# Performance work log

Measured on AMD Instinct MI355X. Metric: run time of the kernel, lower is better.

The kernel has to match this reference:

```python
import jax, jax.numpy as jnp
import numpy as np

K = 2  # top-k experts per token


def setup_inputs() -> dict:
    key = jax.random.key(0)
    k1, k2 = jax.random.split(key)
    B, T, D, E = 4, 4096, 4096, 64
    x = jax.random.normal(k1, (B, T, D), dtype=jnp.float32)
    W = jax.random.normal(k2, (E, D), dtype=jnp.float32) * (1.0 / np.sqrt(D))
    return {"x": x, "W": W}


def reference(x, W):
    # router_logits: [B, T, E]  (nn.Linear with no bias: x @ W.T)
    router_logits = jnp.einsum('btd,ed->bte', x, W)
    # top-k over expert dim, then softmax over the k selected logits
    topk_logits, topk_idx = jax.lax.top_k(router_logits, K)  # [B,T,K]
    topk_weight = jax.nn.softmax(topk_logits, axis=-1)       # [B,T,K]
    return (topk_idx, topk_weight, router_logits)
```

## Files before the change

kernel.cpp:

```cpp
#include <hip/hip_runtime.h>
#include <math.h>

#define NTOK 16384
#define DDIM 4096
#define NEXP 64
#define TAU  2e-4f
#define WS_LO 262144
#define NCW  32

typedef short bf16x8 __attribute__((ext_vector_type(8)));
typedef float f32x4  __attribute__((ext_vector_type(4)));

__device__ __forceinline__ unsigned short bf16_rne(float f) {
  unsigned u = __float_as_uint(f);
  u += 0x7fffu + ((u >> 16) & 1u);
  return (unsigned short)(u >> 16);
}

__device__ __forceinline__ void split4(float4 v, uint2& hi, uint2& lo) {
  unsigned h0 = bf16_rne(v.x), h1 = bf16_rne(v.y), h2 = bf16_rne(v.z), h3 = bf16_rne(v.w);
  float r0 = v.x - __uint_as_float(h0 << 16);
  float r1 = v.y - __uint_as_float(h1 << 16);
  float r2 = v.z - __uint_as_float(h2 << 16);
  float r3 = v.w - __uint_as_float(h3 << 16);
  unsigned l0 = bf16_rne(r0), l1 = bf16_rne(r1), l2 = bf16_rne(r2), l3 = bf16_rne(r3);
  hi = make_uint2(h0 | (h1 << 16), h2 | (h3 << 16));
  lo = make_uint2(l0 | (l1 << 16), l2 | (l3 << 16));
}

__device__ __forceinline__ bf16x8 mk8(uint2 a, uint2 b) {
  union { uint4 u; bf16x8 v; } t;
  t.u = make_uint4(a.x, a.y, b.x, b.y);
  return t.v;
}

__device__ __forceinline__ void gld_lds16(const float* g, char* l) {
  __builtin_amdgcn_global_load_lds((const __attribute__((address_space(1))) void*)g,
                                   (__attribute__((address_space(3))) void*)l,
                                   16, 0, 0);
}

__device__ __forceinline__ bool better(float va, int ia, float vb, int ib) {
  return (va > vb) || (va == vb && ia < ib);
}
__device__ __forceinline__ bool betterd(double va, int ia, double vb, int ib) {
  return (va > vb) || (va == vb && ia < ib);
}
#define CE(va, ia, vb, ib) { if (better(vb, ib, va, ia)) { float _tv = va; va = vb; vb = _tv; int _ti = ia; ia = ib; ib = _ti; } }

__global__ __launch_bounds__(256)
void presplit_w(const float* __restrict__ w, short* __restrict__ ws) {
  const int tid = blockIdx.x * 256 + threadIdx.x;
  const int e = tid >> 9;
  const int o = tid & 511;
  const int c = o >> 2, q = o & 3;
  const int l = (e & 15) + 16 * q;
  const int g = e >> 4;
  const float* src = w + (size_t)e * DDIM + o * 8;
  float4 v0 = *(const float4*)src;
  float4 v1 = *(const float4*)(src + 4);
  uint2 h0, s0, h1, s1;
  split4(v0, h0, s0);
  split4(v1, h1, s1);
  const int off = c * 2048 + g * 512 + l * 8;
  *(uint4*)(ws + off)         = make_uint4(h0.x, h0.y, h1.x, h1.y);
  *(uint4*)(ws + WS_LO + off) = make_uint4(s0.x, s0.y, s1.x, s1.y);
}

__device__ __noinline__ void fixup_token(const float* __restrict__ x,
                                         const float* __restrict__ wgt,
                                         float* __restrict__ out_idx,
                                         float* __restrict__ out_wt,
                                         int tok, unsigned pk, int l) {
  const int e0 = pk & 255, e1 = (pk >> 8) & 255, e2 = (pk >> 16) & 255, e3 = (pk >> 24) & 255;
  const float* xr = x   + (size_t)tok * DDIM + l * 64;
  const float* w0 = wgt + (size_t)e0 * DDIM + l * 64;
  const float* w1 = wgt + (size_t)e1 * DDIM + l * 64;
  const float* w2 = wgt + (size_t)e2 * DDIM + l * 64;
  const float* w3 = wgt + (size_t)e3 * DDIM + l * 64;
  double s0 = 0.0, s1 = 0.0, s2 = 0.0, s3 = 0.0;
#pragma unroll 4
  for (int j = 0; j < 64; j += 4) {
    float4 xv = *(const float4*)(xr + j);
    float4 av = *(const float4*)(w0 + j);
    s0 = fma((double)xv.x, (double)av.x, s0); s0 = fma((double)xv.y, (double)av.y, s0);
    s0 = fma((double)xv.z, (double)av.z, s0); s0 = fma((double)xv.w, (double)av.w, s0);
    av = *(const float4*)(w1 + j);
    s1 = fma((double)xv.x, (double)av.x, s1); s1 = fma((double)xv.y, (double)av.y, s1);
    s1 = fma((double)xv.z, (double)av.z, s1); s1 = fma((double)xv.w, (double)av.w, s1);
    av = *(const float4*)(w2 + j);
    s2 = fma((double)xv.x, (double)av.x, s2); s2 = fma((double)xv.y, (double)av.y, s2);
    s2 = fma((double)xv.z, (double)av.z, s2); s2 = fma((double)xv.w, (double)av.w, s2);
    av = *(const float4*)(w3 + j);
    s3 = fma((double)xv.x, (double)av.x, s3); s3 = fma((double)xv.y, (double)av.y, s3);
    s3 = fma((double)xv.z, (double)av.z, s3); s3 = fma((double)xv.w, (double)av.w, s3);
  }
#pragma unroll
  for (int m = 1; m < 64; m <<= 1) {
    s0 += __shfl_xor(s0, m);
    s1 += __shfl_xor(s1, m);
    s2 += __shfl_xor(s2, m);
    s3 += __shfl_xor(s3, m);
  }
  if (l == 0) {
    double v0 = s0, v1 = s1, v2 = s2, v3 = s3;
    int i0 = e0, i1 = e1, i2 = e2, i3 = e3;
    if (betterd(v1, i1, v0, i0)) { double tv = v0; v0 = v1; v1 = tv; int ti = i0; i0 = i1; i1 = ti; }
    if (betterd(v3, i3, v2, i2)) { double tv = v2; v2 = v3; v3 = tv; int ti = i2; i2 = i3; i3 = ti; }
    if (betterd(v2, i2, v0, i0)) { double tv = v0; v0 = v2; v2 = tv; int ti = i0; i0 = i2; i2 = ti; }
    if (betterd(v3, i3, v1, i1)) { double tv = v1; v1 = v3; v3 = tv; int ti = i1; i1 = i3; i3 = ti; }
    if (betterd(v2, i2, v1, i1)) { double tv = v1; v1 = v2; v2 = tv; int ti = i1; i1 = i2; i2 = ti; }
    double ex = exp(v1 - v0);
    double den = 1.0 + ex;
    out_idx[tok * 2 + 0] = (float)i0;
    out_idx[tok * 2 + 1] = (float)i1;
    out_wt[tok * 2 + 0]  = (float)(1.0 / den);
    out_wt[tok * 2 + 1]  = (float)(ex / den);
  }
}

__global__ __launch_bounds__(256, 2)
void router_main(const float* __restrict__ x, const float* __restrict__ wgt,
                 const short* __restrict__ ws, float* __restrict__ out) {
  __shared__ __align__(16) char ldsbuf[65536];

  const int u = threadIdx.x;
  const int l = u & 63;
  const int wid = u >> 6;
  const int tokBase = blockIdx.x * 32;
  const int row = l & 15;
  const int hq = l >> 4;

  char* ring = ldsbuf + wid * 16384;

  const float* xb0 = x + (size_t)(tokBase +  0 + row) * DDIM + wid * 1024 +  0 + hq * 4;
  const float* xb1 = x + (size_t)(tokBase +  0 + row) * DDIM + wid * 1024 + 16 + hq * 4;
  const float* xb2 = x + (size_t)(tokBase + 16 + row) * DDIM + wid * 1024 +  0 + hq * 4;
  const float* xb3 = x + (size_t)(tokBase + 16 + row) * DDIM + wid * 1024 + 16 + hq * 4;

  const short* whp = ws + wid * 65536 + l * 8;

  const int dsoff = (hq >> 1) * 1024 + ((hq & 1) * 32 + row) * 16;

  f32x4 acc[2][4];
#pragma unroll
  for (int tt = 0; tt < 2; ++tt)
#pragma unroll
    for (int g = 0; g < 4; ++g) acc[tt][g] = (f32x4){0.f, 0.f, 0.f, 0.f};

  bf16x8 whA[4], wlA[4], whB[4], wlB[4];

#define LDW(WH, WL, cc)                                                        \
  { _Pragma("unroll")                                                          \
    for (int g = 0; g < 4; ++g) {                                              \
      WH[g] = *(const bf16x8*)(whp + (cc) * 2048 + g * 512);                   \
      WL[g] = *(const bf16x8*)(whp + WS_LO + (cc) * 2048 + g * 512);           \
    } }

  gld_lds16(xb0, ring);
  gld_lds16(xb1, ring + 1024);
  gld_lds16(xb2, ring + 2048);
  gld_lds16(xb3, ring + 3072);
  asm volatile("" ::: "memory");
  LDW(whA, wlA, 0)
  asm volatile("" ::: "memory");
  gld_lds16(xb0 + 32, ring + 4096);
  gld_lds16(xb1 + 32, ring + 4096 + 1024);
  gld_lds16(xb2 + 32, ring + 4096 + 2048);
  gld_lds16(xb3 + 32, ring + 4096 + 3072);
  asm volatile("" ::: "memory");
  LDW(whB, wlB, 1)

  int slr = 0;
  int slw = 2;

#define STEP(S, WH, WL)                                                        \
  {                                                                            \
    asm volatile("" ::: "memory");                                             \
    const int chx = (S) + 2;                                                   \
    char* xdst = ring + ((chx < NCW) ? slw : 3) * 4096;                        \
    const int xofs = ((chx < NCW) ? chx : (NCW - 1)) * 32;                     \
    gld_lds16(xb0 + xofs, xdst);                                               \
    gld_lds16(xb1 + xofs, xdst + 1024);                                        \
    gld_lds16(xb2 + xofs, xdst + 2048);                                        \
    gld_lds16(xb3 + xofs, xdst + 3072);                                        \
    asm volatile("s_waitcnt vmcnt(16)" ::: "memory");                          \
    const char* rb = ring + slr * 4096;                                        \
    {                                                                          \
      float4 f0 = *(const float4*)(rb + dsoff);                                \
      float4 f1 = *(const float4*)(rb + dsoff + 256);                          \
      uint2 h0, s0, h1, s1;                                                    \
      split4(f0, h0, s0); split4(f1, h1, s1);                                  \
      bf16x8 ahi = mk8(h0, h1), alo = mk8(s0, s1);                             \
      _Pragma("unroll")                                                        \
      for (int g = 0; g < 4; ++g) {                                            \
        acc[0][g] = __builtin_amdgcn_mfma_f32_16x16x32_bf16(ahi, WH[g], acc[0][g], 0, 0, 0); \
        acc[0][g] = __builtin_amdgcn_mfma_f32_16x16x32_bf16(ahi, WL[g], acc[0][g], 0, 0, 0); \
        acc[0][g] = __builtin_amdgcn_mfma_f32_16x16x32_bf16(alo, WH[g], acc[0][g], 0, 0, 0); \
      }                                                                        \
    }                                                                          \
    {                                                                          \
      float4 f0 = *(const float4*)(rb + 2048 + dsoff);                         \
      float4 f1 = *(const float4*)(rb + 2048 + dsoff + 256);                   \
      uint2 h0, s0, h1, s1;                                                    \
      split4(f0, h0, s0); split4(f1, h1, s1);                                  \
      bf16x8 ahi = mk8(h0, h1), alo = mk8(s0, s1);                             \
      _Pragma("unroll")                                                        \
      for (int g = 0; g < 4; ++g) {                                            \
        acc[1][g] = __builtin_amdgcn_mfma_f32_16x16x32_bf16(ahi, WH[g], acc[1][g], 0, 0, 0); \
        acc[1][g] = __builtin_amdgcn_mfma_f32_16x16x32_bf16(ahi, WL[g], acc[1][g], 0, 0, 0); \
        acc[1][g] = __builtin_amdgcn_mfma_f32_16x16x32_bf16(alo, WH[g], acc[1][g], 0, 0, 0); \
      }                                                                        \
    }                                                                          \
    const int chw = ((S) + 2 < NCW) ? (S) + 2 : (NCW - 1);                     \
    asm volatile("" ::: "memory");                                             \
    LDW(WH, WL, chw)                                                           \
    slr = (slr == 2) ? 0 : slr + 1;                                            \
    slw = (slw == 2) ? 0 : slw + 1;                                            \
  }

  for (int s = 0; s < NCW; s += 2) {
    STEP(s, whA, wlA)
    STEP(s + 1, whB, wlB)
  }

  __syncthreads();
  float* p = (float*)ldsbuf;
#define PIDX(KQ, TT, G, R) ((((((KQ) * 2 + (TT)) * 4 + (G)) * 4 + (R)) << 6) + l)
#pragma unroll
  for (int tt = 0; tt < 2; ++tt)
#pragma unroll
    for (int g = 0; g < 4; ++g)
#pragma unroll
      for (int r = 0; r < 4; ++r)
        p[PIDX(wid, tt, g, r)] = acc[tt][g][r];
  __syncthreads();

  float* out_idx = out;
  float* out_wt  = out + NTOK * 2;
  float* out_lg  = out + NTOK * 4;

#pragma unroll
  for (int tt = 0; tt < 2; ++tt) {
    float v0 = p[PIDX(0, tt, 0, wid)] + p[PIDX(1, tt, 0, wid)] + p[PIDX(2, tt, 0, wid)] + p[PIDX(3, tt, 0, wid)];
    float v1 = p[PIDX(0, tt, 1, wid)] + p[PIDX(1, tt, 1, wid)] + p[PIDX(2, tt, 1, wid)] + p[PIDX(3, tt, 1, wid)];
    float v2 = p[PIDX(0, tt, 2, wid)] + p[PIDX(1, tt, 2, wid)] + p[PIDX(2, tt, 2, wid)] + p[PIDX(3, tt, 2, wid)];
    float v3 = p[PIDX(0, tt, 3, wid)] + p[PIDX(1, tt, 3, wid)] + p[PIDX(2, tt, 3, wid)] + p[PIDX(3, tt, 3, wid)];

    const int tok = tokBase + tt * 16 + (l >> 4) * 4 + wid;
    {
      float* dst = out_lg + (size_t)tok * NEXP + (l & 15);
      dst[0]  = v0;
      dst[16] = v1;
      dst[32] = v2;
      dst[48] = v3;
    }

    const int cbase = (l & 15);
    int i0 = cbase, i1 = cbase + 16, i2 = cbase + 32, i3 = cbase + 48;
    CE(v0, i0, v1, i1) CE(v2, i2, v3, i3) CE(v0, i0, v2, i2) CE(v1, i1, v3, i3) CE(v1, i1, v2, i2)
#pragma unroll
    for (int m = 1; m <= 8; m <<= 1) {
      float p0 = __shfl_xor(v0, m), p1 = __shfl_xor(v1, m);
      float p2 = __shfl_xor(v2, m), p3 = __shfl_xor(v3, m);
      int j0 = __shfl_xor(i0, m), j1 = __shfl_xor(i1, m);
      int j2 = __shfl_xor(i2, m), j3 = __shfl_xor(i3, m);
      CE(v0, i0, p3, j3) CE(v1, i1, p2, j2) CE(v2, i2, p1, j1) CE(v3, i3, p0, j0)
      CE(v0, i0, v2, i2) CE(v1, i1, v3, i3) CE(v0, i0, v1, i1) CE(v2, i2, v3, i3)
    }

    bool flag = false;
    unsigned pk = 0;
    if (cbase == 0) {
      flag = (v0 - v1 < TAU) || (v1 - v2 < TAU) || (v2 - v3 < TAU);
      pk = (unsigned)i0 | ((unsigned)i1 << 8) | ((unsigned)i2 << 16) | ((unsigned)i3 << 24);
      if (!flag) {
        float ex = expf(v1 - v0);
        float den = 1.0f + ex;
        out_idx[tok * 2 + 0] = (float)i0;
        out_idx[tok * 2 + 1] = (float)i1;
        out_wt[tok * 2 + 0]  = 1.0f / den;
        out_wt[tok * 2 + 1]  = ex / den;
      }
    }
    unsigned long long mk = __ballot(flag);
    while (mk) {
      const int src = __builtin_ctzll(mk);
      mk &= mk - 1;
      const unsigned pks = (unsigned)__shfl((int)pk, src);
      fixup_token(x, wgt, out_idx, out_wt, tokBase + tt * 16 + (src >> 4) * 4 + wid, pks, l);
    }
  }
}

extern "C" void kernel_launch(void* const* d_in, const int* in_sizes, int n_in,
                              void* d_out, int out_size, void* d_ws, size_t ws_size,
                              hipStream_t stream) {
  const float* x = (const float*)d_in[0];
  const float* w = (const float*)d_in[1];
  float* out = (float*)d_out;
  short* ws = (short*)d_ws;

  hipLaunchKernelGGL(presplit_w, dim3(128), dim3(256), 0, stream, w, ws);
  hipLaunchKernelGGL(router_main, dim3(NTOK / 32), dim3(256), 0, stream, x, w, ws, out);
}
```

Measured before the change: 88.04 us.

## Deepen x/W prefetch pipeline to three chunks and stagger K-start per block

Extends the software pipeline from two to three chunks in flight, using a 4-slot LDS ring and four sets of weight registers, with the wait threshold raised to match. It also rotates each block's starting K chunk by a per-block offset, so concurrent blocks read different parts of W and x at the same moment. The aim is to hide more global-load latency and spread memory traffic across channels. The cost is higher register pressure from the extra weight buffers, which could hurt occupancy under launch_bounds(256,2). Past the end, prefetches wrap around and reload real chunks that are never used.

```diff
diff --git a/kernel.cpp b/kernel.cpp
--- a/kernel.cpp
+++ b/kernel.cpp
@@ -133,6 +133,9 @@
 
   char* ring = ldsbuf + wid * 16384;
 
+  const int P = (blockIdx.x * 13) & 31;
+#define PHYS(T) (((T) + P) & 31)
+
   const float* xb0 = x + (size_t)(tokBase +  0 + row) * DDIM + wid * 1024 +  0 + hq * 4;
   const float* xb1 = x + (size_t)(tokBase +  0 + row) * DDIM + wid * 1024 + 16 + hq * 4;
   const float* xb2 = x + (size_t)(tokBase + 16 + row) * DDIM + wid * 1024 +  0 + hq * 4;
@@ -148,44 +151,42 @@
 #pragma unroll
     for (int g = 0; g < 4; ++g) acc[tt][g] = (f32x4){0.f, 0.f, 0.f, 0.f};
 
-  bf16x8 whA[4], wlA[4], whB[4], wlB[4];
-
-#define LDW(WH, WL, cc)                                                        \
-  { _Pragma("unroll")                                                          \
+  bf16x8 wh0[4], wl0[4], wh1[4], wl1[4], wh2[4], wl2[4], wh3[4], wl3[4];
+
+#define LDW(WH, WL, T)                                                         \
+  { const int cc_ = PHYS(T);                                                   \
+    _Pragma("unroll")                                                          \
     for (int g = 0; g < 4; ++g) {                                              \
-      WH[g] = *(const bf16x8*)(whp + (cc) * 2048 + g * 512);                   \
-      WL[g] = *(const bf16x8*)(whp + WS_LO + (cc) * 2048 + g * 512);           \
+      WH[g] = *(const bf16x8*)(whp + cc_ * 2048 + g * 512);                    \
+      WL[g] = *(const bf16x8*)(whp + WS_LO + cc_ * 2048 + g * 512);            \
     } }
 
-  gld_lds16(xb0, ring);
-  gld_lds16(xb1, ring + 1024);
-  gld_lds16(xb2, ring + 2048);
-  gld_lds16(xb3, ring + 3072);
-  asm volatile("" ::: "memory");
-  LDW(whA, wlA, 0)
-  asm volatile("" ::: "memory");
-  gld_lds16(xb0 + 32, ring + 4096);
-  gld_lds16(xb1 + 32, ring + 4096 + 1024);
-  gld_lds16(xb2 + 32, ring + 4096 + 2048);
-  gld_lds16(xb3 + 32, ring + 4096 + 3072);
-  asm volatile("" ::: "memory");
-  LDW(whB, wlB, 1)
-
-  int slr = 0;
-  int slw = 2;
-
-#define STEP(S, WH, WL)                                                        \
+#define XISSUE(T, SLOT)                                                        \
+  { const int xo_ = PHYS(T) * 32;                                              \
+    char* xd_ = ring + (SLOT) * 4096;                                          \
+    gld_lds16(xb0 + xo_, xd_);                                                 \
+    gld_lds16(xb1 + xo_, xd_ + 1024);                                          \
+    gld_lds16(xb2 + xo_, xd_ + 2048);                                          \
+    gld_lds16(xb3 + xo_, xd_ + 3072); }
+
+  XISSUE(0, 0)
+  asm volatile("" ::: "memory");
+  LDW(wh0, wl0, 0)
+  asm volatile("" ::: "memory");
+  XISSUE(1, 1)
+  asm volatile("" ::: "memory");
+  LDW(wh1, wl1, 1)
+  asm volatile("" ::: "memory");
+  XISSUE(2, 2)
+  asm volatile("" ::: "memory");
+  LDW(wh2, wl2, 2)
+
+#define STEP(T, SR, SW, WHc, WLc, WHn, WLn)                                    \
   {                                                                            \
     asm volatile("" ::: "memory");                                             \
-    const int chx = (S) + 2;                                                   \
-    char* xdst = ring + ((chx < NCW) ? slw : 3) * 4096;                        \
-    const int xofs = ((chx < NCW) ? chx : (NCW - 1)) * 32;                     \
-    gld_lds16(xb0 + xofs, xdst);                                               \
-    gld_lds16(xb1 + xofs, xdst + 1024);                                        \
-    gld_lds16(xb2 + xofs, xdst + 2048);                                        \
-    gld_lds16(xb3 + xofs, xdst + 3072);                                        \
-    asm volatile("s_waitcnt vmcnt(16)" ::: "memory");                          \
-    const char* rb = ring + slr * 4096;                                        \
+    XISSUE((T) + 3, SW)                                                        \
+    asm volatile("s_waitcnt vmcnt(28)" ::: "memory");                          \
+    const char* rb = ring + (SR) * 4096;                                       \
     {                                                                          \
       float4 f0 = *(const float4*)(rb + dsoff);                                \
       float4 f1 = *(const float4*)(rb + dsoff + 256);                          \
@@ -194,9 +195,9 @@
       bf16x8 ahi = mk8(h0, h1), alo = mk8(s0, s1);                             \
       _Pragma("unroll")                                                        \
       for (int g = 0; g < 4; ++g) {                                            \
-        acc[0][g] = __builtin_amdgcn_mfma_f32_16x16x32_bf16(ahi, WH[g], acc[0][g], 0, 0, 0); \
-        acc[0][g] = __builtin_amdgcn_mfma_f32_16x16x32_bf16(ahi, WL[g], acc[0][g], 0, 0, 0); \
-        acc[0][g] = __builtin_amdgcn_mfma_f32_16x16x32_bf16(alo, WH[g], acc[0][g], 0, 0, 0); \
+        acc[0][g] = __builtin_amdgcn_mfma_f32_16x16x32_bf16(ahi, WHc[g], acc[0][g], 0, 0, 0); \
+        acc[0][g] = __builtin_amdgcn_mfma_f32_16x16x32_bf16(ahi, WLc[g], acc[0][g], 0, 0, 0); \
+        acc[0][g] = __builtin_amdgcn_mfma_f32_16x16x32_bf16(alo, WHc[g], acc[0][g], 0, 0, 0); \
       }                                                                        \
     }                                                                          \
     {                                                                          \
@@ -207,21 +208,20 @@
       bf16x8 ahi = mk8(h0, h1), alo = mk8(s0, s1);                             \
       _Pragma("unroll")                                                        \
       for (int g = 0; g < 4; ++g) {                                            \
-        acc[1][g] = __builtin_amdgcn_mfma_f32_16x16x32_bf16(ahi, WH[g], acc[1][g], 0, 0, 0); \
-        acc[1][g] = __builtin_amdgcn_mfma_f32_16x16x32_bf16(ahi, WL[g], acc[1][g], 0, 0, 0); \
-        acc[1][g] = __builtin_amdgcn_mfma_f32_16x16x32_bf16(alo, WH[g], acc[1][g], 0, 0, 0); \
+        acc[1][g] = __builtin_amdgcn_mfma_f32_16x16x32_bf16(ahi, WHc[g], acc[1][g], 0, 0, 0); \
+        acc[1][g] = __builtin_amdgcn_mfma_f32_16x16x32_bf16(ahi, WLc[g], acc[1][g], 0, 0, 0); \
+        acc[1][g] = __builtin_amdgcn_mfma_f32_16x16x32_bf16(alo, WHc[g], acc[1][g], 0, 0, 0); \
       }                                                                        \
     }                                                                          \
-    const int chw = ((S) + 2 < NCW) ? (S) + 2 : (NCW - 1);                     \
     asm volatile("" ::: "memory");                                             \
-    LDW(WH, WL, chw)                                                           \
-    slr = (slr == 2) ? 0 : slr + 1;                                            \
-    slw = (slw == 2) ? 0 : slw + 1;                                            \
-  }
-
-  for (int s = 0; s < NCW; s += 2) {
-    STEP(s, whA, wlA)
-    STEP(s + 1, whB, wlB)
+    LDW(WHn, WLn, (T) + 3)                                                     \
+  }
+
+  for (int t = 0; t < NCW; t += 4) {
+    STEP(t + 0, 0, 3, wh0, wl0, wh3, wl3)
+    STEP(t + 1, 1, 0, wh1, wl1, wh0, wl0)
+    STEP(t + 2, 2, 1, wh2, wl2, wh1, wl1)
+    STEP(t + 3, 3, 2, wh3, wl3, wh2, wl2)
   }
 
   __syncthreads();
```

After: 85.85 us. 2.5% less time.
